# Performance work log

Hardware: AMD Instinct MI355X
Metric: run time of the kernel (lower is better)

The kernel has to match this reference:

```python
import jax, jax.numpy as jnp
import numpy as np

B, T, C = 4, 8192, 1024
H, D = 16, 64  # n_head, head_dim


def setup_inputs() -> dict:
    key = jax.random.key(0)
    ks = jax.random.split(key, 9)
    s = 1.0 / np.sqrt(C)
    return {
        "x": jax.random.normal(ks[0], (B, T, C), jnp.float32),
        "Wq": jax.random.uniform(ks[1], (C, C), jnp.float32, -s, s),
        "bq": jax.random.uniform(ks[2], (C,), jnp.float32, -s, s),
        "Wk": jax.random.uniform(ks[3], (C, C), jnp.float32, -s, s),
        "bk": jax.random.uniform(ks[4], (C,), jnp.float32, -s, s),
        "Wv": jax.random.uniform(ks[5], (C, C), jnp.float32, -s, s),
        "bv": jax.random.uniform(ks[6], (C,), jnp.float32, -s, s),
        "Wp": jax.random.uniform(ks[7], (C, C), jnp.float32, -s, s),
        "bp": jax.random.uniform(ks[8], (C,), jnp.float32, -s, s),
    }


def _heads(t):
    # (B,T,C) -> (B,H,T,D)
    return t.reshape(B, T, H, D).transpose(0, 2, 1, 3)


def reference(x, Wq, bq, Wk, bk, Wv, bv, Wp, bp):
    q = _heads(x @ Wq.T + bq)
    k = _heads(x @ Wk.T + bk)
    v = _heads(x @ Wv.T + bv)
    # attn_type='l1': softmax q,k over feature dim; L1 normalizer
    q = jax.nn.softmax(q, axis=-1)
    k = jax.nn.softmax(k, axis=-1)
    k_sum = k.sum(axis=-2, keepdims=True)               # (B,H,1,D)
    D_inv = 1.0 / (q * k_sum).sum(axis=-1, keepdims=True)  # (B,H,T,1)
    context = jnp.einsum('bhtd,bhte->bhde', k, v)       # (B,H,D,D)
    out = jnp.einsum('bhtd,bhde->bhte', q, context) * D_inv + q
    out = out.transpose(0, 2, 1, 3).reshape(B, T, C)
    return out @ Wp.T + bp
```

## Files before the change

### kernel.cpp

```cpp
#include <hip/hip_runtime.h>
#include <hip/hip_bf16.h>
#include <stdint.h>


#define BT    32768
#define CDIM  1024

using bf16 = __hip_bfloat16;
typedef short  short8   __attribute__((ext_vector_type(8)));
typedef short  short4_t __attribute__((ext_vector_type(4)));
typedef unsigned short ushort4_t __attribute__((ext_vector_type(4)));
typedef float  floatx4  __attribute__((ext_vector_type(4)));

__device__ __forceinline__ float bfbits2f(unsigned short u) {
    union { unsigned int i; float f; } c; c.i = ((unsigned int)u) << 16; return c.f;
}

__device__ __forceinline__ void gld_lds16(const void* g, void* lds) {
    __builtin_amdgcn_global_load_lds(
        (const __attribute__((address_space(1))) uint32_t*)g,
        (__attribute__((address_space(3))) uint32_t*)lds,
        16, 0, 0);
}

__global__ void zero_kernel(float* __restrict__ p) {
    p[(size_t)blockIdx.x * 256 + threadIdx.x] = 0.0f;
}

__global__ void cvt_kernel(const float* __restrict__ x,
                           const float* __restrict__ Wq, const float* __restrict__ Wk,
                           const float* __restrict__ Wv, const float* __restrict__ Wp,
                           bf16* __restrict__ xb, bf16* __restrict__ Wb) {
    const int XF4 = (BT * CDIM) / 4;
    int i = blockIdx.x * 256 + threadIdx.x;
    const float* src; bf16* dst; int off;
    if (i < XF4) { src = x; dst = xb; off = i; }
    else {
        int i2 = i - XF4;
        int wi = i2 >> 18;
        off = i2 & 0x3FFFF;
        src = (wi == 0) ? Wq : (wi == 1) ? Wk : (wi == 2) ? Wv : Wp;
        dst = Wb + (size_t)wi * 1048576;
    }
    float4 f = ((const float4*)src)[off];
    union { bf16 h[4]; short4_t v; } u;
    u.h[0] = __float2bfloat16(f.x); u.h[1] = __float2bfloat16(f.y);
    u.h[2] = __float2bfloat16(f.z); u.h[3] = __float2bfloat16(f.w);
    *(short4_t*)(dst + (size_t)off * 4) = u.v;
}

__global__ __launch_bounds__(256)
void gemm_qkv(const bf16* __restrict__ A, const bf16* __restrict__ Bw,
              const float* __restrict__ bq, const float* __restrict__ bk,
              const float* __restrict__ bv,
              bf16* __restrict__ qb, bf16* __restrict__ kb, bf16* __restrict__ vb) {
    __shared__ bf16 sA[128 * 32];
    __shared__ bf16 sB[128 * 32];
    int tid = threadIdx.x, lane = tid & 63, wv = tid >> 6;
    int bn = blockIdx.x % 24;
    int bm = blockIdx.x / 24;
    const bf16* Ab = A  + (size_t)bm * 128 * CDIM;
    const bf16* Bb = Bw + (size_t)bn * 128 * CDIM;
    int srow = lane >> 2, scol = (lane & 3) * 8;

    floatx4 acc[4][4] = {};
    int quad = lane >> 4, l15 = lane & 15;
    int m0 = (wv & 1) * 64, n0v = (wv >> 1) * 64;

    for (int kt = 0; kt < 32; ++kt) {
        int k0 = kt * 32;
        #pragma unroll
        for (int c = 0; c < 2; ++c) {
            int chunk = wv * 2 + c;
            gld_lds16(Ab + (size_t)(chunk * 16 + srow) * CDIM + k0 + scol, &sA[chunk * 512]);
            gld_lds16(Bb + (size_t)(chunk * 16 + srow) * CDIM + k0 + scol, &sB[chunk * 512]);
        }
        __syncthreads();
        short8 af[4], bfr[4];
        #pragma unroll
        for (int i = 0; i < 4; ++i) {
            af[i]  = *(const short8*)&sA[(m0  + i * 16 + l15) * 32 + quad * 8];
            bfr[i] = *(const short8*)&sB[(n0v + i * 16 + l15) * 32 + quad * 8];
        }
        #pragma unroll
        for (int i = 0; i < 4; ++i)
            #pragma unroll
            for (int j = 0; j < 4; ++j)
                acc[i][j] = __builtin_amdgcn_mfma_f32_16x16x32_bf16(af[i], bfr[j], acc[i][j], 0, 0, 0);
        __syncthreads();
    }

    int grow0 = bm * 128 + m0;
    int n_abs = bn * 128 + n0v;
    bf16* dst; const float* biasp; int ncol0; bool smax;
    if (n_abs < 1024)      { dst = qb; biasp = bq; ncol0 = n_abs;        smax = true;  }
    else if (n_abs < 2048) { dst = kb; biasp = bk; ncol0 = n_abs - 1024; smax = true;  }
    else                   { dst = vb; biasp = bv; ncol0 = n_abs - 2048; smax = false; }
    float bias4[4];
    #pragma unroll
    for (int j = 0; j < 4; ++j) bias4[j] = biasp[ncol0 + j * 16 + l15];

    #pragma unroll
    for (int i = 0; i < 4; ++i) {
        #pragma unroll
        for (int r = 0; r < 4; ++r) {
            float vals[4];
            #pragma unroll
            for (int j = 0; j < 4; ++j) vals[j] = acc[i][j][r] + bias4[j];
            if (smax) {
                float mx = fmaxf(fmaxf(vals[0], vals[1]), fmaxf(vals[2], vals[3]));
                #pragma unroll
                for (int d = 1; d < 16; d <<= 1) mx = fmaxf(mx, __shfl_xor(mx, d));
                float s = 0.f;
                #pragma unroll
                for (int j = 0; j < 4; ++j) { vals[j] = __expf(vals[j] - mx); s += vals[j]; }
                #pragma unroll
                for (int d = 1; d < 16; d <<= 1) s += __shfl_xor(s, d);
                float rinv = 1.0f / s;
                #pragma unroll
                for (int j = 0; j < 4; ++j) vals[j] *= rinv;
            }
            size_t row = (size_t)(grow0 + i * 16 + quad * 4 + r);
            #pragma unroll
            for (int j = 0; j < 4; ++j)
                dst[row * 1024 + ncol0 + j * 16 + l15] = __float2bfloat16(vals[j]);
        }
    }
}

__global__ __launch_bounds__(256)
void ctx_kernel(const bf16* __restrict__ kbuf, const bf16* __restrict__ vbuf,
                float* __restrict__ ctx, float* __restrict__ ksum) {
    int bid = blockIdx.x;
    int head = bid >> 3, chunk = bid & 7;
    int b = head >> 4, h = head & 15;
    size_t rowbase = (size_t)b * 8192 + (size_t)chunk * 1024;
    int coff = h * 64;
    __shared__ bf16 ks[64 * 64];
    __shared__ bf16 vs[64 * 64];
    int tid = threadIdx.x;
    int lrow = tid >> 2, lpart = tid & 3;
    int di = tid >> 4, ei = tid & 15;

    float acc[16];
    #pragma unroll
    for (int i = 0; i < 16; ++i) acc[i] = 0.f;
    float ksv[4] = {0.f, 0.f, 0.f, 0.f};

    size_t gbase = (rowbase + lrow) * 1024 + coff + lpart * 16;
    short8 pk0 = *(const short8*)(kbuf + gbase);
    short8 pk1 = *(const short8*)(kbuf + gbase + 8);
    short8 pv0 = *(const short8*)(vbuf + gbase);
    short8 pv1 = *(const short8*)(vbuf + gbase + 8);

    for (int st = 0; st < 16; ++st) {
        __syncthreads();
        *(short8*)&ks[lrow * 64 + lpart * 16]     = pk0;
        *(short8*)&ks[lrow * 64 + lpart * 16 + 8] = pk1;
        *(short8*)&vs[lrow * 64 + lpart * 16]     = pv0;
        *(short8*)&vs[lrow * 64 + lpart * 16 + 8] = pv1;
        __syncthreads();
        if (st < 15) {
            size_t g = gbase + (size_t)(st + 1) * 64 * 1024;
            pk0 = *(const short8*)(kbuf + g);
            pk1 = *(const short8*)(kbuf + g + 8);
            pv0 = *(const short8*)(vbuf + g);
            pv1 = *(const short8*)(vbuf + g + 8);
        }
        for (int t = 0; t < 64; ++t) {
            ushort4_t ku = *(const ushort4_t*)&ks[t * 64 + di * 4];
            ushort4_t vu = *(const ushort4_t*)&vs[t * 64 + ei * 4];
            float kd[4], ve[4];
            #pragma unroll
            for (int i = 0; i < 4; ++i) { kd[i] = bfbits2f(ku[i]); ve[i] = bfbits2f(vu[i]); }
            #pragma unroll
            for (int i = 0; i < 4; ++i)
                #pragma unroll
                for (int j = 0; j < 4; ++j)
                    acc[i * 4 + j] = fmaf(kd[i], ve[j], acc[i * 4 + j]);
            #pragma unroll
            for (int j = 0; j < 4; ++j) ksv[j] += kd[j];
        }
    }
    float* cptr = ctx + (size_t)head * 4096;
    #pragma unroll
    for (int i = 0; i < 4; ++i)
        #pragma unroll
        for (int j = 0; j < 4; ++j)
            atomicAdd(&cptr[(di * 4 + i) * 64 + ei * 4 + j], acc[i * 4 + j]);
    if (ei == 0) {
        #pragma unroll
        for (int j = 0; j < 4; ++j) atomicAdd(&ksum[head * 64 + di * 4 + j], ksv[j]);
    }
}

__global__ __launch_bounds__(256)
void attn_kernel(const bf16* __restrict__ qbuf, const float* __restrict__ ctx,
                 const float* __restrict__ ksum, bf16* __restrict__ ab) {
    int bid = blockIdx.x;
    int head = bid >> 7, tb = bid & 127;
    int b = head >> 4, h = head & 15;
    size_t row0 = (size_t)b * 8192 + (size_t)tb * 64;
    int coff = h * 64;
    __shared__ bf16 qs[64 * 80];
    __shared__ bf16 cts[64 * 80];
    __shared__ float ksums[64];
    __shared__ float dinv[64];
    int tid = threadIdx.x, lane = tid & 63, wv = tid >> 6;

    {
        int lrow = tid >> 2, lpart = tid & 3;
        size_t g = (row0 + lrow) * 1024 + coff + lpart * 16;
        short8 q0 = *(const short8*)(qbuf + g);
        short8 q1 = *(const short8*)(qbuf + g + 8);
        *(short8*)&qs[lrow * 80 + lpart * 16]     = q0;
        *(short8*)&qs[lrow * 80 + lpart * 16 + 8] = q1;
    }
    {
        const float* cp = ctx + (size_t)head * 4096;
        #pragma unroll
        for (int it = 0; it < 4; ++it) {
            int fi = it * 256 + tid;
            int d = fi >> 4, e0 = (fi & 15) * 4;
            float4 f = ((const float4*)cp)[fi];
            cts[(e0 + 0) * 80 + d] = __float2bfloat16(f.x);
            cts[(e0 + 1) * 80 + d] = __float2bfloat16(f.y);
            cts[(e0 + 2) * 80 + d] = __float2bfloat16(f.z);
            cts[(e0 + 3) * 80 + d] = __float2bfloat16(f.w);
        }
    }
    if (tid < 64) ksums[tid] = ksum[head * 64 + tid];
    __syncthreads();

    {
        int t = tid >> 2, dg = tid & 3;
        float p = 0.f;
        #pragma unroll
        for (int j = 0; j < 16; ++j)
            p = fmaf(__bfloat162float(qs[t * 80 + dg * 16 + j]), ksums[dg * 16 + j], p);
        p += __shfl_xor(p, 1);
        p += __shfl_xor(p, 2);
        if (dg == 0) dinv[t] = 1.0f / p;
    }
    __syncthreads();

    int quad = lane >> 4, l15 = lane & 15;
    int trow0 = wv * 16;
    short8 aF0 = *(const short8*)&qs[(trow0 + l15) * 80 + quad * 8];
    short8 aF1 = *(const short8*)&qs[(trow0 + l15) * 80 + 32 + quad * 8];
    floatx4 acc[4] = {};
    #pragma unroll
    for (int ni = 0; ni < 4; ++ni) {
        short8 b0 = *(const short8*)&cts[(ni * 16 + l15) * 80 + quad * 8];
        short8 b1 = *(const short8*)&cts[(ni * 16 + l15) * 80 + 32 + quad * 8];
        acc[ni] = __builtin_amdgcn_mfma_f32_16x16x32_bf16(aF0, b0, acc[ni], 0, 0, 0);
        acc[ni] = __builtin_amdgcn_mfma_f32_16x16x32_bf16(aF1, b1, acc[ni], 0, 0, 0);
    }
    float dv[4];
    #pragma unroll
    for (int r = 0; r < 4; ++r) dv[r] = dinv[trow0 + quad * 4 + r];
    #pragma unroll
    for (int ni = 0; ni < 4; ++ni) {
        #pragma unroll
        for (int r = 0; r < 4; ++r) {
            int row = trow0 + quad * 4 + r;
            int col = ni * 16 + l15;
            float val = acc[ni][r] * dv[r] + __bfloat162float(qs[row * 80 + col]);
            ab[(row0 + row) * 1024 + coff + col] = __float2bfloat16(val);
        }
    }
}

__global__ __launch_bounds__(256)
void gemm_out(const bf16* __restrict__ A, const bf16* __restrict__ Bw,
              const float* __restrict__ bp, float* __restrict__ outp) {
    __shared__ bf16 sA[128 * 32];
    __shared__ bf16 sB[128 * 32];
    int tid = threadIdx.x, lane = tid & 63, wv = tid >> 6;
    int bn = blockIdx.x & 7;
    int bm = blockIdx.x >> 3;
    const bf16* Ab = A  + (size_t)bm * 128 * CDIM;
    const bf16* Bb = Bw + (size_t)bn * 128 * CDIM;
    int srow = lane >> 2, scol = (lane & 3) * 8;
    floatx4 acc[4][4] = {};
    int quad = lane >> 4, l15 = lane & 15;
    int m0 = (wv & 1) * 64, n0v = (wv >> 1) * 64;

    for (int kt = 0; kt < 32; ++kt) {
        int k0 = kt * 32;
        #pragma unroll
        for (int c = 0; c < 2; ++c) {
            int chunk = wv * 2 + c;
            gld_lds16(Ab + (size_t)(chunk * 16 + srow) * CDIM + k0 + scol, &sA[chunk * 512]);
            gld_lds16(Bb + (size_t)(chunk * 16 + srow) * CDIM + k0 + scol, &sB[chunk * 512]);
        }
        __syncthreads();
        short8 af[4], bfr[4];
        #pragma unroll
        for (int i = 0; i < 4; ++i) {
            af[i]  = *(const short8*)&sA[(m0  + i * 16 + l15) * 32 + quad * 8];
            bfr[i] = *(const short8*)&sB[(n0v + i * 16 + l15) * 32 + quad * 8];
        }
        #pragma unroll
        for (int i = 0; i < 4; ++i)
            #pragma unroll
            for (int j = 0; j < 4; ++j)
                acc[i][j] = __builtin_amdgcn_mfma_f32_16x16x32_bf16(af[i], bfr[j], acc[i][j], 0, 0, 0);
        __syncthreads();
    }
    int grow0 = bm * 128 + m0;
    int gcol0 = bn * 128 + n0v;
    float bias4[4];
    #pragma unroll
    for (int j = 0; j < 4; ++j) bias4[j] = bp[gcol0 + j * 16 + l15];
    #pragma unroll
    for (int i = 0; i < 4; ++i)
        #pragma unroll
        for (int r = 0; r < 4; ++r) {
            size_t row = (size_t)(grow0 + i * 16 + quad * 4 + r);
            #pragma unroll
            for (int j = 0; j < 4; ++j)
                outp[row * 1024 + gcol0 + j * 16 + l15] = acc[i][j][r] + bias4[j];
        }
}

extern "C" void kernel_launch(void* const* d_in, const int* in_sizes, int n_in,
                              void* d_out, int out_size, void* d_ws, size_t ws_size,
                              hipStream_t stream) {
    const float* x  = (const float*)d_in[0];
    const float* Wq = (const float*)d_in[1];
    const float* bq = (const float*)d_in[2];
    const float* Wk = (const float*)d_in[3];
    const float* bk = (const float*)d_in[4];
    const float* Wv = (const float*)d_in[5];
    const float* bv = (const float*)d_in[6];
    const float* Wp = (const float*)d_in[7];
    const float* bp = (const float*)d_in[8];
    float* outp = (float*)d_out;

    char* ws = (char*)d_ws;
    bf16*  xb   = (bf16*)(ws);
    bf16*  Wb   = (bf16*)(ws + 67108864);
    bf16*  qb   = (bf16*)(ws + 75497472);
    bf16*  kb   = (bf16*)(ws + 142606336);
    bf16*  vb   = (bf16*)(ws + 209715200);
    float* ctx  = (float*)(ws + 276824064);
    float* ksum = (float*)(ws + 277872640);
    bf16*  ab   = (bf16*)(ws);

    zero_kernel<<<1040, 256, 0, stream>>>(ctx);
    cvt_kernel<<<36864, 256, 0, stream>>>(x, Wq, Wk, Wv, Wp, xb, Wb);
    gemm_qkv<<<6144, 256, 0, stream>>>(xb, Wb, bq, bk, bv, qb, kb, vb);
    ctx_kernel<<<512, 256, 0, stream>>>(kb, vb, ctx, ksum);
    attn_kernel<<<8192, 256, 0, stream>>>(qb, ctx, ksum, ab);
    gemm_out<<<2048, 256, 0, stream>>>(ab, Wb + (size_t)3072 * 1024, bp, outp);
}
```

Measured before the change: 743.4 us.

## Swizzle GEMM LDS tiles, split ctx kernel finer, shrink attn LDS padding

Applies an XOR swizzle to the LDS column position in both GEMM kernels, on the global_load_lds write side and the MFMA fragment read side, to reduce LDS bank conflicts. Doubles the ctx_kernel grid to 1024 blocks, each covering 512 rows instead of 1024, so more CUs have work, at the cost of twice as many atomic adds into ctx. Changes the attn_kernel LDS row stride from 80 to 72 elements to alter bank mapping and reduce shared memory use.

Result: faster. 726.2 us (-2.3%).

```diff
diff --git a/kernel.cpp b/kernel.cpp
--- a/kernel.cpp
+++ b/kernel.cpp
@@ -61,11 +61,13 @@
     int bm = blockIdx.x / 24;
     const bf16* Ab = A  + (size_t)bm * 128 * CDIM;
     const bf16* Bb = Bw + (size_t)bn * 128 * CDIM;
-    int srow = lane >> 2, scol = (lane & 3) * 8;
+    int srow = lane >> 2;
+    int scol = ((lane & 3) ^ ((lane >> 3) & 3)) * 8;
 
     floatx4 acc[4][4] = {};
     int quad = lane >> 4, l15 = lane & 15;
     int m0 = (wv & 1) * 64, n0v = (wv >> 1) * 64;
+    int rpos = (quad ^ ((l15 >> 1) & 3)) * 8;
 
     for (int kt = 0; kt < 32; ++kt) {
         int k0 = kt * 32;
@@ -79,8 +81,8 @@
         short8 af[4], bfr[4];
         #pragma unroll
         for (int i = 0; i < 4; ++i) {
-            af[i]  = *(const short8*)&sA[(m0  + i * 16 + l15) * 32 + quad * 8];
-            bfr[i] = *(const short8*)&sB[(n0v + i * 16 + l15) * 32 + quad * 8];
+            af[i]  = *(const short8*)&sA[(m0  + i * 16 + l15) * 32 + rpos];
+            bfr[i] = *(const short8*)&sB[(n0v + i * 16 + l15) * 32 + rpos];
         }
         #pragma unroll
         for (int i = 0; i < 4; ++i)
@@ -132,9 +134,9 @@
 void ctx_kernel(const bf16* __restrict__ kbuf, const bf16* __restrict__ vbuf,
                 float* __restrict__ ctx, float* __restrict__ ksum) {
     int bid = blockIdx.x;
-    int head = bid >> 3, chunk = bid & 7;
+    int head = bid >> 4, chunk = bid & 15;
     int b = head >> 4, h = head & 15;
-    size_t rowbase = (size_t)b * 8192 + (size_t)chunk * 1024;
+    size_t rowbase = (size_t)b * 8192 + (size_t)chunk * 512;
     int coff = h * 64;
     __shared__ bf16 ks[64 * 64];
     __shared__ bf16 vs[64 * 64];
@@ -153,14 +155,14 @@
     short8 pv0 = *(const short8*)(vbuf + gbase);
     short8 pv1 = *(const short8*)(vbuf + gbase + 8);
 
-    for (int st = 0; st < 16; ++st) {
+    for (int st = 0; st < 8; ++st) {
         __syncthreads();
         *(short8*)&ks[lrow * 64 + lpart * 16]     = pk0;
         *(short8*)&ks[lrow * 64 + lpart * 16 + 8] = pk1;
         *(short8*)&vs[lrow * 64 + lpart * 16]     = pv0;
         *(short8*)&vs[lrow * 64 + lpart * 16 + 8] = pv1;
         __syncthreads();
-        if (st < 15) {
+        if (st < 7) {
             size_t g = gbase + (size_t)(st + 1) * 64 * 1024;
             pk0 = *(const short8*)(kbuf + g);
             pk1 = *(const short8*)(kbuf + g + 8);
@@ -194,6 +196,7 @@
     }
 }
 
+#define QS 72
 __global__ __launch_bounds__(256)
 void attn_kernel(const bf16* __restrict__ qbuf, const float* __restrict__ ctx,
                  const float* __restrict__ ksum, bf16* __restrict__ ab) {
@@ -202,8 +205,8 @@
     int b = head >> 4, h = head & 15;
     size_t row0 = (size_t)b * 8192 + (size_t)tb * 64;
     int coff = h * 64;
-    __shared__ bf16 qs[64 * 80];
-    __shared__ bf16 cts[64 * 80];
+    __shared__ bf16 qs[64 * QS];
+    __shared__ bf16 cts[64 * QS];
     __shared__ float ksums[64];
     __shared__ float dinv[64];
     int tid = threadIdx.x, lane = tid & 63, wv = tid >> 6;
@@ -213,8 +216,8 @@
         size_t g = (row0 + lrow) * 1024 + coff + lpart * 16;
         short8 q0 = *(const short8*)(qbuf + g);
         short8 q1 = *(const short8*)(qbuf + g + 8);
-        *(short8*)&qs[lrow * 80 + lpart * 16]     = q0;
-        *(short8*)&qs[lrow * 80 + lpart * 16 + 8] = q1;
+        *(short8*)&qs[lrow * QS + lpart * 16]     = q0;
+        *(short8*)&qs[lrow * QS + lpart * 16 + 8] = q1;
     }
     {
         const float* cp = ctx + (size_t)head * 4096;
@@ -223,10 +226,10 @@
             int fi = it * 256 + tid;
             int d = fi >> 4, e0 = (fi & 15) * 4;
             float4 f = ((const float4*)cp)[fi];
-            cts[(e0 + 0) * 80 + d] = __float2bfloat16(f.x);
-            cts[(e0 + 1) * 80 + d] = __float2bfloat16(f.y);
-            cts[(e0 + 2) * 80 + d] = __float2bfloat16(f.z);
-            cts[(e0 + 3) * 80 + d] = __float2bfloat16(f.w);
+            cts[(e0 + 0) * QS + d] = __float2bfloat16(f.x);
+            cts[(e0 + 1) * QS + d] = __float2bfloat16(f.y);
+            cts[(e0 + 2) * QS + d] = __float2bfloat16(f.z);
+            cts[(e0 + 3) * QS + d] = __float2bfloat16(f.w);
         }
     }
     if (tid < 64) ksums[tid] = ksum[head * 64 + tid];
@@ -237,7 +240,7 @@
         float p = 0.f;
         #pragma unroll
         for (int j = 0; j < 16; ++j)
-            p = fmaf(__bfloat162float(qs[t * 80 + dg * 16 + j]), ksums[dg * 16 + j], p);
+            p = fmaf(__bfloat162float(qs[t * QS + dg * 16 + j]), ksums[dg * 16 + j], p);
         p += __shfl_xor(p, 1);
         p += __shfl_xor(p, 2);
         if (dg == 0) dinv[t] = 1.0f / p;
@@ -246,13 +249,13 @@
 
     int quad = lane >> 4, l15 = lane & 15;
     int trow0 = wv * 16;
-    short8 aF0 = *(const short8*)&qs[(trow0 + l15) * 80 + quad * 8];
-    short8 aF1 = *(const short8*)&qs[(trow0 + l15) * 80 + 32 + quad * 8];
+    short8 aF0 = *(const short8*)&qs[(trow0 + l15) * QS + quad * 8];
+    short8 aF1 = *(const short8*)&qs[(trow0 + l15) * QS + 32 + quad * 8];
     floatx4 acc[4] = {};
     #pragma unroll
     for (int ni = 0; ni < 4; ++ni) {
-        short8 b0 = *(const short8*)&cts[(ni * 16 + l15) * 80 + quad * 8];
-        short8 b1 = *(const short8*)&cts[(ni * 16 + l15) * 80 + 32 + quad * 8];
+        short8 b0 = *(const short8*)&cts[(ni * 16 + l15) * QS + quad * 8];
+        short8 b1 = *(const short8*)&cts[(ni * 16 + l15) * QS + 32 + quad * 8];
         acc[ni] = __builtin_amdgcn_mfma_f32_16x16x32_bf16(aF0, b0, acc[ni], 0, 0, 0);
         acc[ni] = __builtin_amdgcn_mfma_f32_16x16x32_bf16(aF1, b1, acc[ni], 0, 0, 0);
     }
@@ -265,7 +268,7 @@
         for (int r = 0; r < 4; ++r) {
             int row = trow0 + quad * 4 + r;
             int col = ni * 16 + l15;
-            float val = acc[ni][r] * dv[r] + __bfloat162float(qs[row * 80 + col]);
+            float val = acc[ni][r] * dv[r] + __bfloat162float(qs[row * QS + col]);
             ab[(row0 + row) * 1024 + coff + col] = __float2bfloat16(val);
         }
     }
@@ -281,10 +284,12 @@
     int bm = blockIdx.x >> 3;
     const bf16* Ab = A  + (size_t)bm * 128 * CDIM;
     const bf16* Bb = Bw + (size_t)bn * 128 * CDIM;
-    int srow = lane >> 2, scol = (lane & 3) * 8;
+    int srow = lane >> 2;
+    int scol = ((lane & 3) ^ ((lane >> 3) & 3)) * 8;
     floatx4 acc[4][4] = {};
     int quad = lane >> 4, l15 = lane & 15;
     int m0 = (wv & 1) * 64, n0v = (wv >> 1) * 64;
+    int rpos = (quad ^ ((l15 >> 1) & 3)) * 8;
 
     for (int kt = 0; kt < 32; ++kt) {
         int k0 = kt * 32;
@@ -298,8 +303,8 @@
         short8 af[4], bfr[4];
         #pragma unroll
         for (int i = 0; i < 4; ++i) {
-            af[i]  = *(const short8*)&sA[(m0  + i * 16 + l15) * 32 + quad * 8];
-            bfr[i] = *(const short8*)&sB[(n0v + i * 16 + l15) * 32 + quad * 8];
+            af[i]  = *(const short8*)&sA[(m0  + i * 16 + l15) * 32 + rpos];
+            bfr[i] = *(const short8*)&sB[(n0v + i * 16 + l15) * 32 + rpos];
         }
         #pragma unroll
         for (int i = 0; i < 4; ++i)
@@ -351,7 +356,7 @@
     zero_kernel<<<1040, 256, 0, stream>>>(ctx);
     cvt_kernel<<<36864, 256, 0, stream>>>(x, Wq, Wk, Wv, Wp, xb, Wb);
     gemm_qkv<<<6144, 256, 0, stream>>>(xb, Wb, bq, bk, bv, qb, kb, vb);
-    ctx_kernel<<<512, 256, 0, stream>>>(kb, vb, ctx, ksum);
+    ctx_kernel<<<1024, 256, 0, stream>>>(kb, vb, ctx, ksum);
     attn_kernel<<<8192, 256, 0, stream>>>(qb, ctx, ksum, ab);
     gemm_out<<<2048, 256, 0, stream>>>(ab, Wb + (size_t)3072 * 1024, bp, outp);
 }
```
